# Kernel optimization log

Hardware: AMD Instinct MI355X
Metric: run time of the kernel (lower is better)

## Reference

```python
import jax, jax.numpy as jnp
import numpy as np
import math

B, L, D, H = 8, 2048, 1024, 16
DK = D // H
FACTOR = 1
TOP_K = int(FACTOR * math.log(L))  # = 7


def _linear(x, W, b):
    # torch nn.Linear: y = x @ W.T + b, W shape (out, in)
    return x @ W.T + b


def setup_inputs() -> dict:
    rng = jax.random.key(0)
    ks = jax.random.split(rng, 11)
    s = 1.0 / math.sqrt(D)
    inp = {
        "query": jax.random.normal(ks[0], (B, L, D), jnp.float32),
        "key": jax.random.normal(ks[1], (B, L, D), jnp.float32),
        "value": jax.random.normal(ks[2], (B, L, D), jnp.float32),
        "Wq": jax.random.normal(ks[3], (D, D), jnp.float32) * s,
        "bq": jnp.zeros((D,), jnp.float32),
        "Wk": jax.random.normal(ks[4], (D, D), jnp.float32) * s,
        "bk": jnp.zeros((D,), jnp.float32),
        "Wv": jax.random.normal(ks[5], (D, D), jnp.float32) * s,
        "bv": jnp.zeros((D,), jnp.float32),
        "Wo": jax.random.normal(ks[6], (D, D), jnp.float32) * s,
        "bo": jnp.zeros((D,), jnp.float32),
    }
    return inp


def _autocorrelation(q, k, v):
    # q,k,v: (B, H, DK, L)
    q_fft = jnp.fft.rfft(q, axis=-1)
    k_fft = jnp.fft.rfft(k, axis=-1)
    corr = jnp.fft.irfft(q_fft * jnp.conj(k_fft), n=L, axis=-1)  # (B,H,DK,L)

    mean_value = jnp.mean(corr, axis=2)                 # (B,H,L)
    weights, index = jax.lax.top_k(mean_value, TOP_K)   # (B,H,TOP_K)
    tmp_corr = jax.nn.softmax(weights, axis=-1)         # (B,H,TOP_K)

    t = jnp.arange(L)[None, None, :]                    # (1,1,L)
    delays_agg = jnp.zeros_like(v)
    for i in range(TOP_K):  # TOP_K=7, static small loop
        # torch.roll(v, -delay, -1)[..., t] == v[..., (t+delay) % L]
        idx = (t + index[:, :, i:i + 1]) % L            # (B,H,L)
        idx = jnp.broadcast_to(idx[:, :, None, :], v.shape)
        pattern = jnp.take_along_axis(v, idx, axis=-1)  # (B,H,DK,L)
        delays_agg = delays_agg + pattern * tmp_corr[:, :, i][:, :, None, None]
    return delays_agg, tmp_corr


def reference(query, key, value, Wq, bq, Wk, bk, Wv, bv, Wo, bo):
    residual = query
    # project and split heads -> (B, H, DK, L)
    q = _linear(query, Wq, bq).reshape(B, L, H, DK).transpose(0, 2, 3, 1)
    k = _linear(key, Wk, bk).reshape(B, L, H, DK).transpose(0, 2, 3, 1)
    v = _linear(value, Wv, bv).reshape(B, L, H, DK).transpose(0, 2, 3, 1)

    agg, corr_weights = _autocorrelation(q, k, v)       # (B,H,DK,L)
    corr_value = agg.transpose(0, 3, 1, 2).reshape(B, L, D)
    corr_value = _linear(corr_value, Wo, bo)
    # dropout in eval mode = identity
    return corr_value + residual, corr_weights
```

## Files before the change

kernel.cpp:

```cpp
#include <hip/hip_runtime.h>
#include <hip/hip_bf16.h>
#include <math.h>

#define BB   8
#define LL   2048
#define DD   1024
#define HH   16
#define DKK  64
#define TOPK 7

typedef unsigned short u16;
typedef short short8 __attribute__((ext_vector_type(8)));
typedef short s4v    __attribute__((ext_vector_type(4)));
typedef float f32x4  __attribute__((ext_vector_type(4)));
typedef int   int4v  __attribute__((ext_vector_type(4)));

#define QXH_B   0ull
#define QXL_B   16777216ull
#define KXH_B   33554432ull
#define KXL_B   50331648ull
#define VXH_B   67108864ull
#define QWH_B   100663296ull
#define QWL_B   101711872ull
#define KWH_B   102760448ull
#define KWL_B   103809024ull
#define VWH_B   104857600ull
#define OWH_B   106954752ull
#define QTB_B   109051904ull
#define KTB_B   142606336ull
#define VBF_B   176160768ull
#define PART_B  0ull
#define PART_STRIDE 2064
#define TOPW_B  16777216ull
#define TOPI_B  16780800ull

#define SX_INV  5461.3333f
#define SW_INV  174762.67f
#define CS1     6.8664551e-5f
#define CS2     2.6822090e-7f

__device__ __forceinline__ int2 xcd_swizzle_8x128() {
    const int lin = blockIdx.y * gridDim.x + blockIdx.x;
    const int swz = (lin & 7) * 128 + (lin >> 3);
    return make_int2(swz & 7, swz >> 3);
}

__device__ __forceinline__ u16 f2bf(float f) {
    unsigned u = __float_as_uint(f);
    unsigned r = u + 0x7FFFu + ((u >> 16) & 1u);
    return (u16)(r >> 16);
}
__device__ __forceinline__ float bf2f(u16 h) {
    return __uint_as_float((unsigned)h << 16);
}

__device__ __forceinline__ void split4_i8(const float* __restrict__ x,
                                          char* __restrict__ hi,
                                          char* __restrict__ lo,
                                          float inv_s, size_t i) {
    float4 t = ((const float4*)x)[i];
    float f[4] = {t.x, t.y, t.z, t.w};
    unsigned hp = 0, lp = 0;
    #pragma unroll
    for (int j = 0; j < 4; ++j) {
        int q = __float2int_rn(f[j] * inv_s);
        q = min(max(q, -32639), 32639);
        int xl = ((q + 128) & 255) - 128;
        int xh = (q - xl) >> 8;
        hp |= ((unsigned)(xh & 255)) << (8 * j);
        lp |= ((unsigned)(xl & 255)) << (8 * j);
    }
    ((unsigned*)hi)[i] = hp;
    ((unsigned*)lo)[i] = lp;
}

__device__ __forceinline__ void cvt4_bf(const float* __restrict__ x,
                                        u16* __restrict__ o, size_t i) {
    float4 t = ((const float4*)x)[i];
    s4v h;
    h[0] = (short)f2bf(t.x); h[1] = (short)f2bf(t.y);
    h[2] = (short)f2bf(t.z); h[3] = (short)f2bf(t.w);
    *(s4v*)(o + i * 4) = h;
}

__global__ __launch_bounds__(256) void k_conv_all(
    const float* __restrict__ q, const float* __restrict__ k,
    const float* __restrict__ v,
    const float* __restrict__ Wq, const float* __restrict__ Wk,
    const float* __restrict__ Wv, const float* __restrict__ Wo,
    char* __restrict__ qh, char* __restrict__ ql,
    char* __restrict__ kh, char* __restrict__ kl, u16* __restrict__ vx,
    char* __restrict__ qwh, char* __restrict__ qwl,
    char* __restrict__ kwh, char* __restrict__ kwl,
    u16* __restrict__ vwh, u16* __restrict__ owh)
{
    const int b = blockIdx.x;
    const int t = threadIdx.x;
    if (b < 16384) {
        split4_i8(q, qh, ql, SX_INV, (size_t)b * 256 + t);
    } else if (b < 32768) {
        split4_i8(k, kh, kl, SX_INV, (size_t)(b - 16384) * 256 + t);
    } else if (b < 49152) {
        cvt4_bf(v, vx, (size_t)(b - 32768) * 256 + t);
    } else if (b < 50176) {
        split4_i8(Wq, qwh, qwl, SW_INV, (size_t)(b - 49152) * 256 + t);
    } else if (b < 51200) {
        split4_i8(Wk, kwh, kwl, SW_INV, (size_t)(b - 50176) * 256 + t);
    } else if (b < 52224) {
        cvt4_bf(Wv, vwh, (size_t)(b - 51200) * 256 + t);
    } else {
        cvt4_bf(Wo, owh, (size_t)(b - 52224) * 256 + t);
    }
}

__device__ __forceinline__ void async16(u16* l, const u16* g) {
    __builtin_amdgcn_global_load_lds(
        (const __attribute__((address_space(1))) void*)g,
        (__attribute__((address_space(3))) void*)l, 16, 0, 0);
}
__device__ __forceinline__ void async16b(char* l, const char* g) {
    __builtin_amdgcn_global_load_lds(
        (const __attribute__((address_space(1))) void*)g,
        (__attribute__((address_space(3))) void*)l, 16, 0, 0);
}

__global__ __launch_bounds__(256, 2) void gemm_i8split(
    const char* __restrict__ Ah, const char* __restrict__ Al,
    const char* __restrict__ Bh, const char* __restrict__ Bl,
    const float* __restrict__ bias, u16* __restrict__ outb)
{
    __shared__ __align__(16) char lds[2][4][8192];
    const int t = threadIdx.x;
    const int w = t >> 6, lane = t & 63;
    const int2 tb = xcd_swizzle_8x128();
    const int m0 = tb.y * 128, n0 = tb.x * 128;
    const int srow = lane >> 2, sslot = lane & 3;
    const int r15 = lane & 15, kg = lane >> 4;
    const int wr = w >> 1, wc = w & 1;
    const int r4 = (lane >> 4) * 4;
    const int swzb = (kg ^ (r15 & 3)) << 4;
    const int a_off = (wr * 64 + r15) * 64 + swzb;
    const int b_off = (wc * 64 + r15) * 64 + swzb;

    int4v acc1[4][4], acc2[4][4];
    #pragma unroll
    for (int i = 0; i < 4; ++i)
        #pragma unroll
        for (int j = 0; j < 4; ++j) {
            acc1[i][j] = (int4v){0,0,0,0};
            acc2[i][j] = (int4v){0,0,0,0};
        }

    #define STAGE8(buf, kt)                                                       \
    {                                                                             \
        const int gc0 = (kt) * 64;                                                \
        _Pragma("unroll")                                                         \
        for (int i = 0; i < 2; ++i) {                                             \
            const int row  = w * 32 + i * 16 + srow;                              \
            const int kch  = (sslot ^ (row & 3)) << 4;                            \
            const int loff = w * 2048 + i * 1024;                                 \
            async16b(&lds[buf][0][loff], Ah + (size_t)(m0 + row) * 1024 + gc0 + kch); \
            async16b(&lds[buf][1][loff], Bh + (size_t)(n0 + row) * 1024 + gc0 + kch); \
            async16b(&lds[buf][2][loff], Al + (size_t)(m0 + row) * 1024 + gc0 + kch); \
            async16b(&lds[buf][3][loff], Bl + (size_t)(n0 + row) * 1024 + gc0 + kch); \
        }                                                                         \
    }

    #define COMP8(buf)                                                            \
    {                                                                             \
        const char* cb = &lds[buf][0][0];                                         \
        int4v ah[4], bh4[4], al[4], bl[4];                                        \
        _Pragma("unroll")                                                         \
        for (int mi = 0; mi < 4; ++mi) ah[mi] = *(const int4v*)(cb + a_off + mi * 1024); \
        _Pragma("unroll")                                                         \
        for (int nj = 0; nj < 4; ++nj) bh4[nj] = *(const int4v*)(cb + 8192 + b_off + nj * 1024); \
        _Pragma("unroll")                                                         \
        for (int mi = 0; mi < 4; ++mi)                                            \
            _Pragma("unroll")                                                     \
            for (int nj = 0; nj < 4; ++nj)                                        \
                acc1[mi][nj] = __builtin_amdgcn_mfma_i32_16x16x64_i8(ah[mi], bh4[nj], acc1[mi][nj], 0, 0, 0); \
        _Pragma("unroll")                                                         \
        for (int nj = 0; nj < 4; ++nj) bl[nj] = *(const int4v*)(cb + 24576 + b_off + nj * 1024); \
        _Pragma("unroll")                                                         \
        for (int mi = 0; mi < 4; ++mi)                                            \
            _Pragma("unroll")                                                     \
            for (int nj = 0; nj < 4; ++nj)                                        \
                acc2[mi][nj] = __builtin_amdgcn_mfma_i32_16x16x64_i8(ah[mi], bl[nj], acc2[mi][nj], 0, 0, 0); \
        _Pragma("unroll")                                                         \
        for (int mi = 0; mi < 4; ++mi) al[mi] = *(const int4v*)(cb + 16384 + a_off + mi * 1024); \
        _Pragma("unroll")                                                         \
        for (int mi = 0; mi < 4; ++mi)                                            \
            _Pragma("unroll")                                                     \
            for (int nj = 0; nj < 4; ++nj)                                        \
                acc2[mi][nj] = __builtin_amdgcn_mfma_i32_16x16x64_i8(al[mi], bh4[nj], acc2[mi][nj], 0, 0, 0); \
    }

    STAGE8(0, 0);
    __syncthreads();
    int cur = 0;
    for (int kt = 0; kt < 15; ++kt) {
        STAGE8(cur ^ 1, kt + 1);
        COMP8(cur);
        __syncthreads();
        cur ^= 1;
    }
    COMP8(cur);

    #pragma unroll
    for (int nj = 0; nj < 4; ++nj) {
        const int n = n0 + wc * 64 + nj * 16 + r15;
        const float bs = bias[n];
        #pragma unroll
        for (int mi = 0; mi < 4; ++mi) {
            const int m = m0 + wr * 64 + mi * 16 + r4;
            const int b = m >> 11;
            const int l = m & 2047;
            s4v v;
            #pragma unroll
            for (int r = 0; r < 4; ++r)
                v[r] = (short)f2bf(fmaf(CS1, (float)acc1[mi][nj][r],
                                   fmaf(CS2, (float)acc2[mi][nj][r], bs)));
            *(s4v*)(outb + (((size_t)((b << 10) + n)) << 11) + l) = v;
        }
    }
    #undef STAGE8
    #undef COMP8
}

template<int EPI>
__global__ __launch_bounds__(512, 2) void gemm_bf16_256(
    const u16* __restrict__ A, const u16* __restrict__ B,
    const float* __restrict__ bias, const float* __restrict__ resid,
    float* __restrict__ outp)
{
    extern __shared__ u16 ldsx[];
    u16* lsA = ldsx;
    u16* lsB = ldsx + 32768;
    const int t = threadIdx.x;
    const int wid = t >> 6, lane = t & 63;
    const int wr = wid >> 2, wc = wid & 3;
    const int r15 = lane & 15, kg = lane >> 4, r4 = kg * 4;
    const int lin = blockIdx.y * gridDim.x + blockIdx.x;
    const int swz = (lin & 7) * 32 + (lin >> 3);
    const int n0 = (swz & 3) * 256, m0 = (swz >> 2) * 256;
    const int sb = wid * 2;
    const int sr = lane >> 3;
    const int ss = lane & 7;

    #define STG(bufb, ls, rb, src, base0, kt)                                   \
    {                                                                           \
        _Pragma("unroll")                                                       \
        for (int j = 0; j < 2; ++j) {                                           \
            const int r = (rb) + (sb + j) * 8 + sr;                             \
            async16(ls + (size_t)(bufb) * 16384 + (size_t)(rb) * 64 + (size_t)(sb + j) * 512, \
                    src + (size_t)((base0) + r) * 1024 + (kt) * 64 + ((ss ^ (r & 7)) << 3)); \
        }                                                                       \
    }

    f32x4 acc[8][4];
    #pragma unroll
    for (int i = 0; i < 8; ++i)
        #pragma unroll
        for (int j = 0; j < 4; ++j)
            acc[i][j] = (f32x4){0.f, 0.f, 0.f, 0.f};

    STG(0, lsB, 0,   B, n0, 0);
    STG(0, lsB, 128, B, n0, 0);
    STG(0, lsA, 0,   A, m0, 0);
    STG(0, lsA, 128, A, m0, 0);

    for (int kt = 0; kt < 16; ++kt) {
        const int bf = kt & 1, nb = bf ^ 1;
        asm volatile("s_waitcnt vmcnt(0)" ::: "memory");
        asm volatile("s_barrier" ::: "memory");
        short8 bfr[4][2];
        #pragma unroll
        for (int nj = 0; nj < 4; ++nj)
            #pragma unroll
            for (int ks = 0; ks < 2; ++ks) {
                const int row = wc * 64 + nj * 16 + r15;
                bfr[nj][ks] = *(const short8*)(lsB + (size_t)bf * 16384 +
                    (size_t)row * 64 + ((((ks << 2) + kg) ^ (row & 7)) << 3));
            }
        #pragma unroll
        for (int p = 0; p < 4; ++p) {
            short8 afr[2][2];
            #pragma unroll
            for (int mh = 0; mh < 2; ++mh)
                #pragma unroll
                for (int ks = 0; ks < 2; ++ks) {
                    const int row = wr * 128 + (p * 2 + mh) * 16 + r15;
                    afr[mh][ks] = *(const short8*)(lsA + (size_t)bf * 16384 +
                        (size_t)row * 64 + ((((ks << 2) + kg) ^ (row & 7)) << 3));
                }
            if (kt < 15) {
                if (p == 0)      { STG(nb, lsB, 0,   B, n0, kt + 1); }
                else if (p == 1) { STG(nb, lsB, 128, B, n0, kt + 1); }
                else if (p == 2) { STG(nb, lsA, 0,   A, m0, kt + 1); }
                else             { STG(nb, lsA, 128, A, m0, kt + 1); }
            }
            asm volatile("s_barrier" ::: "memory");
            __builtin_amdgcn_s_setprio(1);
            #pragma unroll
            for (int mh = 0; mh < 2; ++mh)
                #pragma unroll
                for (int nj = 0; nj < 4; ++nj)
                    #pragma unroll
                    for (int ks = 0; ks < 2; ++ks)
                        acc[p * 2 + mh][nj] = __builtin_amdgcn_mfma_f32_16x16x32_bf16(
                            afr[mh][ks], bfr[nj][ks], acc[p * 2 + mh][nj], 0, 0, 0);
            __builtin_amdgcn_s_setprio(0);
            asm volatile("s_barrier" ::: "memory");
        }
    }

    if (EPI == 2) {
        u16* outb = (u16*)outp;
        #pragma unroll
        for (int nj = 0; nj < 4; ++nj) {
            const int n = n0 + wc * 64 + nj * 16 + r15;
            const float bs = bias[n];
            #pragma unroll
            for (int mi = 0; mi < 8; ++mi) {
                const int m = m0 + wr * 128 + mi * 16 + r4;
                const int b = m >> 11;
                const int l = m & 2047;
                s4v v;
                #pragma unroll
                for (int r = 0; r < 4; ++r) v[r] = (short)f2bf(acc[mi][nj][r] + bs);
                *(s4v*)(outb + (((size_t)((b << 10) + n)) << 11) + l) = v;
            }
        }
    } else {
        #pragma unroll
        for (int mi = 0; mi < 8; ++mi) {
            #pragma unroll
            for (int r = 0; r < 4; ++r) {
                const int m = m0 + wr * 128 + mi * 16 + r4 + r;
                const float* rrow = resid + ((size_t)m << 10);
                float* orow = outp + ((size_t)m << 10);
                #pragma unroll
                for (int nj = 0; nj < 4; ++nj) {
                    const int n = n0 + wc * 64 + nj * 16 + r15;
                    orow[n] = acc[mi][nj][r] + bias[n] + rrow[n];
                }
            }
        }
    }
    #undef STG
}

#define IDX(i) ((i) + ((i) >> 3))
#define FFT_BUF 2304

__device__ __forceinline__ float2 c_add(float2 a, float2 b){ return make_float2(a.x+b.x, a.y+b.y); }
__device__ __forceinline__ float2 c_sub(float2 a, float2 b){ return make_float2(a.x-b.x, a.y-b.y); }
__device__ __forceinline__ float2 cmul(float2 a, float2 b){
    return make_float2(fmaf(a.x, b.x, -a.y*b.y), fmaf(a.x, b.y, a.y*b.x));
}
template<bool INV>
__device__ __forceinline__ float2 rot90(float2 z) {
    return INV ? make_float2(-z.y, z.x) : make_float2(z.y, -z.x);
}

template<bool INV>
__device__ __forceinline__ void dft8(const float2* a, float2* y) {
    const float r = 0.70710678118654752f;
    float2 e0 = c_add(a[0], a[4]), e1 = c_sub(a[0], a[4]);
    float2 e2 = c_add(a[2], a[6]), e3 = rot90<INV>(c_sub(a[2], a[6]));
    float2 E0 = c_add(e0, e2), E2 = c_sub(e0, e2);
    float2 E1 = c_add(e1, e3), E3 = c_sub(e1, e3);
    float2 o0 = c_add(a[1], a[5]), o1 = c_sub(a[1], a[5]);
    float2 o2 = c_add(a[3], a[7]), o3 = rot90<INV>(c_sub(a[3], a[7]));
    float2 O0 = c_add(o0, o2), O2 = c_sub(o0, o2);
    float2 O1 = c_add(o1, o3), O3 = c_sub(o1, o3);
    float2 T1 = INV ? make_float2(r*(O1.x - O1.y), r*(O1.x + O1.y))
                    : make_float2(r*(O1.x + O1.y), r*(O1.y - O1.x));
    float2 T2 = rot90<INV>(O2);
    float2 T3 = INV ? make_float2(-r*(O3.x + O3.y), r*(O3.x - O3.y))
                    : make_float2(r*(O3.y - O3.x), -r*(O3.x + O3.y));
    y[0] = c_add(E0, O0); y[4] = c_sub(E0, O0);
    y[1] = c_add(E1, T1); y[5] = c_sub(E1, T1);
    y[2] = c_add(E2, T2); y[6] = c_sub(E2, T2);
    y[3] = c_add(E3, T3); y[7] = c_sub(E3, T3);
}

template<bool INV>
__device__ float2* fft2048_r8(float2* bufA, float2* bufB, const float2* twd, int tid)
{
    float2* src = bufA;
    float2* dst = bufB;
    #pragma unroll
    for (int st = 0; st < 3; ++st) {
        const int s = 1 << (3 * st);
        const int u = tid;
        const int sp = u & ~(s - 1);
        float2 a[8], y[8];
        #pragma unroll
        for (int t = 0; t < 8; ++t) a[t] = src[IDX(u + (t << 8))];
        dft8<INV>(a, y);
        float2 w1 = twd[sp];
        if (INV) w1.y = -w1.y;
        const int ob = u + 7 * sp;
        dst[IDX(ob)]     = y[0];
        dst[IDX(ob + s)] = cmul(y[1], w1);
        float2 w = w1;
        #pragma unroll
        for (int t = 2; t < 8; ++t) {
            w = cmul(w, w1);
            dst[IDX(ob + t * s)] = cmul(y[t], w);
        }
        __syncthreads();
        float2* tmp = src; src = dst; dst = tmp;
    }
    #pragma unroll
    for (int h = 0; h < 2; ++h) {
        const int u = tid + (h << 8);
        float2 a0 = src[IDX(u)],        a1 = src[IDX(u + 512)];
        float2 a2 = src[IDX(u + 1024)], a3 = src[IDX(u + 1536)];
        float2 b0 = c_add(a0, a2), b1 = c_sub(a0, a2);
        float2 b2 = c_add(a1, a3), b3 = rot90<INV>(c_sub(a1, a3));
        dst[IDX(u)]        = c_add(b0, b2);
        dst[IDX(u + 512)]  = c_add(b1, b3);
        dst[IDX(u + 1024)] = c_sub(b0, b2);
        dst[IDX(u + 1536)] = c_sub(b1, b3);
    }
    __syncthreads();
    return dst;
}

__global__ __launch_bounds__(256) void fft_corr_partial(
    const u16* __restrict__ qT, const u16* __restrict__ kT,
    float* __restrict__ part)
{
    __shared__ float2 bufA[FFT_BUF];
    __shared__ float2 bufB[FFT_BUF];
    __shared__ float2 twd[256];
    const int tid = threadIdx.x;
    const int blk = blockIdx.x;
    const int bh  = blk >> 3, g = blk & 7;
    {
        float s, c;
        sincosf((float)tid * 3.0679615757712823e-3f, &s, &c);
        twd[tid] = make_float2(c, -s);
    }
    float2 racc[4];
    #pragma unroll
    for (int ii = 0; ii < 4; ++ii) racc[ii] = make_float2(0.f, 0.f);
    float2 racc4 = make_float2(0.f, 0.f);

    const u16* qbase = qT + ((size_t)bh * DKK + g * 8) * LL;
    const u16* kbase = kT + ((size_t)bh * DKK + g * 8) * LL;
    for (int dd = 0; dd < 8; ++dd) {
        __syncthreads();
        const u16* qr = qbase + (size_t)dd * LL;
        const u16* kr = kbase + (size_t)dd * LL;
        short8 q8 = *(const short8*)(qr + tid * 8);
        short8 k8 = *(const short8*)(kr + tid * 8);
        #pragma unroll
        for (int j = 0; j < 8; ++j)
            bufA[IDX(tid * 8 + j)] = make_float2(bf2f((u16)q8[j]), bf2f((u16)k8[j]));
        __syncthreads();
        float2* res = fft2048_r8<false>(bufA, bufB, twd, tid);
        #pragma unroll
        for (int ii = 0; ii < 4; ++ii) {
            const int f = tid + (ii << 8);
            float2 zf = res[IDX(f)];
            float2 zc = res[IDX((2048 - f) & 2047)];
            float2 Q = make_float2(0.5f*(zf.x + zc.x), 0.5f*(zf.y - zc.y));
            float2 K = make_float2(0.5f*(zf.y + zc.y), -0.5f*(zf.x - zc.x));
            racc[ii].x += Q.x*K.x + Q.y*K.y;
            racc[ii].y += Q.y*K.x - Q.x*K.y;
        }
        if (tid == 0) {
            float2 zf = res[IDX(1024)];
            racc4.x += zf.x * zf.y;
        }
    }
    float* po = part + (size_t)blk * PART_STRIDE;
    #pragma unroll
    for (int ii = 0; ii < 4; ++ii) {
        const int f = tid + (ii << 8);
        po[2*f]     = racc[ii].x;
        po[2*f + 1] = racc[ii].y;
    }
    if (tid == 0) { po[2048] = racc4.x; po[2049] = racc4.y; }
}

__global__ __launch_bounds__(256) void fft_inv_topk(
    const float* __restrict__ part, float* __restrict__ out1,
    float* __restrict__ topw, int* __restrict__ topi)
{
    __shared__ float2 bufA[FFT_BUF];
    __shared__ float2 bufB[FFT_BUF];
    __shared__ float2 twd[256];
    __shared__ float  mv[2048];
    __shared__ float  rv[256];
    __shared__ int    ri[256];
    __shared__ float  selv[TOPK];
    __shared__ int    seli[TOPK];
    const int tid = threadIdx.x;
    const int bh  = blockIdx.x;
    {
        float s, c;
        sincosf((float)tid * 3.0679615757712823e-3f, &s, &c);
        twd[tid] = make_float2(c, -s);
    }
    for (int f = tid; f < 1025; f += 256) {
        float sx = 0.f, sy = 0.f;
        for (int g2 = 0; g2 < 8; ++g2) {
            const float* po = part + (size_t)(bh * 8 + g2) * PART_STRIDE + 2*f;
            sx += po[0]; sy += po[1];
        }
        bufA[IDX(f)] = make_float2(sx, sy);
        if (f > 0 && f < 1024) bufA[IDX(2048 - f)] = make_float2(sx, -sy);
    }
    __syncthreads();
    float2* res = fft2048_r8<true>(bufA, bufB, twd, tid);
    const float scale = 1.0f / (2048.0f * 64.0f);
    #pragma unroll
    for (int j = 0; j < 8; ++j) {
        const int l = tid + (j << 8);
        mv[l] = res[IDX(l)].x * scale;
    }
    __syncthreads();
    for (int it = 0; it < TOPK; ++it) {
        float bvv = -3.0e38f; int bii = 0;
        #pragma unroll
        for (int c = 0; c < 8; ++c) {
            const int idx = tid * 8 + c;
            const float v = mv[idx];
            if (v > bvv) { bvv = v; bii = idx; }
        }
        rv[tid] = bvv; ri[tid] = bii;
        __syncthreads();
        for (int off = 128; off > 0; off >>= 1) {
            if (tid < off) {
                const float v2 = rv[tid + off]; const int i2 = ri[tid + off];
                if (v2 > rv[tid] || (v2 == rv[tid] && i2 < ri[tid])) {
                    rv[tid] = v2; ri[tid] = i2;
                }
            }
            __syncthreads();
        }
        if (tid == 0) { selv[it] = rv[0]; seli[it] = ri[0]; mv[ri[0]] = -3.0e38f; }
        __syncthreads();
    }
    if (tid == 0) {
        const float mx = selv[0];
        float e[TOPK]; float ssum = 0.f;
        #pragma unroll
        for (int i = 0; i < TOPK; ++i) { e[i] = expf(selv[i] - mx); ssum += e[i]; }
        const float inv = 1.0f / ssum;
        #pragma unroll
        for (int i = 0; i < TOPK; ++i) {
            const float w = e[i] * inv;
            out1[bh * TOPK + i] = w;
            topw[bh * TOPK + i] = w;
            topi[bh * TOPK + i] = seli[i];
        }
    }
}

__global__ __launch_bounds__(256) void gather_tr(
    const u16* __restrict__ vbf, const float* __restrict__ topw,
    const int* __restrict__ topi, u16* __restrict__ aggrow)
{
    extern __shared__ u16 vstage[];
    __shared__ float wv[TOPK];
    __shared__ int   wi[TOPK];
    const int blk  = blockIdx.x;
    const int bh   = blk >> 1, half = blk & 1;
    const int b    = bh >> 4, h = bh & 15;
    const int tid  = threadIdx.x;
    if (tid < TOPK) {
        wv[tid] = topw[bh * TOPK + tid];
        wi[tid] = topi[bh * TOPK + tid];
    }
    const u16* vsrc = vbf + ((size_t)bh * DKK + half * 32) * LL;
    short8* vs8 = (short8*)vstage;
    #pragma unroll
    for (int k = 0; k < 32; ++k)
        vs8[tid + k * 256] = *(const short8*)(vsrc + (size_t)(tid + k * 256) * 8);
    __syncthreads();
    const int doff = h * 64 + half * 32;
    for (int c = 0; c < 8; ++c) {
        const int l = c * 256 + tid;
        u16* orow = aggrow + ((size_t)((b << 11) + l) << 10) + doff;
        short8 o[4];
        #pragma unroll
        for (int d = 0; d < 32; ++d) {
            float s = 0.f;
            #pragma unroll
            for (int i = 0; i < TOPK; ++i)
                s = fmaf(wv[i], bf2f(vstage[d * 2048 + ((l + wi[i]) & 2047)]), s);
            o[d >> 3][d & 7] = (short)f2bf(s);
        }
        #pragma unroll
        for (int q = 0; q < 4; ++q)
            *(short8*)(orow + q * 8) = o[q];
    }
}

extern "C" void kernel_launch(void* const* d_in, const int* in_sizes, int n_in,
                              void* d_out, int out_size, void* d_ws, size_t ws_size,
                              hipStream_t stream)
{
    const float* query = (const float*)d_in[0];
    const float* key   = (const float*)d_in[1];
    const float* value = (const float*)d_in[2];
    const float* Wq    = (const float*)d_in[3];
    const float* bq    = (const float*)d_in[4];
    const float* Wk    = (const float*)d_in[5];
    const float* bk    = (const float*)d_in[6];
    const float* Wv    = (const float*)d_in[7];
    const float* bv    = (const float*)d_in[8];
    const float* Wo    = (const float*)d_in[9];
    const float* bo    = (const float*)d_in[10];
    float* out = (float*)d_out;
    char*  ws  = (char*)d_ws;

    char* qxh = (char*)(ws + QXH_B);
    char* qxl = (char*)(ws + QXL_B);
    char* kxh = (char*)(ws + KXH_B);
    char* kxl = (char*)(ws + KXL_B);
    u16*  vxh = (u16*)(ws + VXH_B);
    char* qwh = (char*)(ws + QWH_B);
    char* qwl = (char*)(ws + QWL_B);
    char* kwh = (char*)(ws + KWH_B);
    char* kwl = (char*)(ws + KWL_B);
    u16*  vwh = (u16*)(ws + VWH_B);
    u16*  owh = (u16*)(ws + OWH_B);
    u16*  qTb = (u16*)(ws + QTB_B);
    u16*  kTb = (u16*)(ws + KTB_B);
    u16*  vbf = (u16*)(ws + VBF_B);
    float* part = (float*)(ws + PART_B);
    float* topw = (float*)(ws + TOPW_B);
    int*   topi = (int*)(ws + TOPI_B);
    u16*  aggrow = (u16*)(ws + QTB_B);

    dim3 gg(DD / 128, (BB * LL) / 128);
    dim3 g2(DD / 256, (BB * LL) / 256);

    k_conv_all<<<53248, 256, 0, stream>>>(query, key, value, Wq, Wk, Wv, Wo,
                                          qxh, qxl, kxh, kxl, vxh,
                                          qwh, qwl, kwh, kwl, vwh, owh);
    gemm_i8split<<<gg, 256, 0, stream>>>(qxh, qxl, qwh, qwl, bq, qTb);
    gemm_i8split<<<gg, 256, 0, stream>>>(kxh, kxl, kwh, kwl, bk, kTb);
    gemm_bf16_256<2><<<g2, 512, 131072, stream>>>(vxh, vwh, bv, nullptr, (float*)vbf);
    fft_corr_partial<<<BB * HH * 8, 256, 0, stream>>>(qTb, kTb, part);
    fft_inv_topk<<<BB * HH, 256, 0, stream>>>(part, out + 16777216, topw, topi);
    gather_tr<<<BB * HH * 2, 256, 131072, stream>>>(vbf, topw, topi, aggrow);
    gemm_bf16_256<1><<<g2, 512, 131072, stream>>>(aggrow, owh, bo, query, out);
}
```

Baseline: 363.7 us.

## Enlarge int8 split GEMM tile to 256x128 with 8 waves and interleaved staging

The Q and K projection int8-split GEMM now uses 256x128 tiles with 512 threads in place of 128x128 tiles with 256 threads, so each B tile is reused across more rows. The main loop is rewritten to split the three MFMA phases with barriers, issue the next-stage async loads between them, and raise wave priority around the MFMA blocks. This is meant to improve operand reuse and overlap of loads with compute. In exchange it needs 96KB of dynamic LDS, adds many more barriers per iteration, and launches fewer blocks.

```diff
diff --git a/kernel.cpp b/kernel.cpp
--- a/kernel.cpp
+++ b/kernel.cpp
@@ -39,12 +39,6 @@
 #define CS1     6.8664551e-5f
 #define CS2     2.6822090e-7f
 
-__device__ __forceinline__ int2 xcd_swizzle_8x128() {
-    const int lin = blockIdx.y * gridDim.x + blockIdx.x;
-    const int swz = (lin & 7) * 128 + (lin >> 3);
-    return make_int2(swz & 7, swz >> 3);
-}
-
 __device__ __forceinline__ u16 f2bf(float f) {
     unsigned u = __float_as_uint(f);
     unsigned r = u + 0x7FFFu + ((u >> 16) & 1u);
@@ -124,23 +118,30 @@
         (__attribute__((address_space(3))) void*)l, 16, 0, 0);
 }
 
-__global__ __launch_bounds__(256, 2) void gemm_i8split(
+__global__ __launch_bounds__(512, 2) void gemm_i8_256(
     const char* __restrict__ Ah, const char* __restrict__ Al,
     const char* __restrict__ Bh, const char* __restrict__ Bl,
     const float* __restrict__ bias, u16* __restrict__ outb)
 {
-    __shared__ __align__(16) char lds[2][4][8192];
+    extern __shared__ char ldsc[];
+    char* lAh = ldsc;
+    char* lAl = ldsc + 32768;
+    char* lBh = ldsc + 65536;
+    char* lBl = ldsc + 81920;
     const int t = threadIdx.x;
-    const int w = t >> 6, lane = t & 63;
-    const int2 tb = xcd_swizzle_8x128();
-    const int m0 = tb.y * 128, n0 = tb.x * 128;
-    const int srow = lane >> 2, sslot = lane & 3;
-    const int r15 = lane & 15, kg = lane >> 4;
-    const int wr = w >> 1, wc = w & 1;
-    const int r4 = (lane >> 4) * 4;
-    const int swzb = (kg ^ (r15 & 3)) << 4;
-    const int a_off = (wr * 64 + r15) * 64 + swzb;
-    const int b_off = (wc * 64 + r15) * 64 + swzb;
+    const int wid = t >> 6, lane = t & 63;
+    const int wr = wid >> 1, wc = wid & 1;
+    const int r15 = lane & 15, kg = lane >> 4, r4 = kg * 4;
+    const int lin = blockIdx.y * gridDim.x + blockIdx.x;
+    const int swz = (lin & 7) * 64 + (lin >> 3);
+    const int n0 = (swz & 7) * 128, m0 = (swz >> 3) * 256;
+
+    #define STGU(ls, bufb, bufsz, rowbase, src, base0, kt)                      \
+    {                                                                           \
+        const int r = (rowbase) + wid * 16 + (lane >> 2);                       \
+        async16b(ls + (size_t)(bufb) * (bufsz) + (size_t)(rowbase) * 64 + wid * 1024, \
+                 src + (size_t)((base0) + r) * 1024 + (kt) * 64 + (((lane & 3) ^ (r & 3)) << 4)); \
+    }
 
     int4v acc1[4][4], acc2[4][4];
     #pragma unroll
@@ -151,60 +152,87 @@
             acc2[i][j] = (int4v){0,0,0,0};
         }
 
-    #define STAGE8(buf, kt)                                                       \
-    {                                                                             \
-        const int gc0 = (kt) * 64;                                                \
-        _Pragma("unroll")                                                         \
-        for (int i = 0; i < 2; ++i) {                                             \
-            const int row  = w * 32 + i * 16 + srow;                              \
-            const int kch  = (sslot ^ (row & 3)) << 4;                            \
-            const int loff = w * 2048 + i * 1024;                                 \
-            async16b(&lds[buf][0][loff], Ah + (size_t)(m0 + row) * 1024 + gc0 + kch); \
-            async16b(&lds[buf][1][loff], Bh + (size_t)(n0 + row) * 1024 + gc0 + kch); \
-            async16b(&lds[buf][2][loff], Al + (size_t)(m0 + row) * 1024 + gc0 + kch); \
-            async16b(&lds[buf][3][loff], Bl + (size_t)(n0 + row) * 1024 + gc0 + kch); \
-        }                                                                         \
-    }
-
-    #define COMP8(buf)                                                            \
-    {                                                                             \
-        const char* cb = &lds[buf][0][0];                                         \
-        int4v ah[4], bh4[4], al[4], bl[4];                                        \
-        _Pragma("unroll")                                                         \
-        for (int mi = 0; mi < 4; ++mi) ah[mi] = *(const int4v*)(cb + a_off + mi * 1024); \
-        _Pragma("unroll")                                                         \
-        for (int nj = 0; nj < 4; ++nj) bh4[nj] = *(const int4v*)(cb + 8192 + b_off + nj * 1024); \
-        _Pragma("unroll")                                                         \
-        for (int mi = 0; mi < 4; ++mi)                                            \
-            _Pragma("unroll")                                                     \
-            for (int nj = 0; nj < 4; ++nj)                                        \
-                acc1[mi][nj] = __builtin_amdgcn_mfma_i32_16x16x64_i8(ah[mi], bh4[nj], acc1[mi][nj], 0, 0, 0); \
-        _Pragma("unroll")                                                         \
-        for (int nj = 0; nj < 4; ++nj) bl[nj] = *(const int4v*)(cb + 24576 + b_off + nj * 1024); \
-        _Pragma("unroll")                                                         \
-        for (int mi = 0; mi < 4; ++mi)                                            \
-            _Pragma("unroll")                                                     \
-            for (int nj = 0; nj < 4; ++nj)                                        \
-                acc2[mi][nj] = __builtin_amdgcn_mfma_i32_16x16x64_i8(ah[mi], bl[nj], acc2[mi][nj], 0, 0, 0); \
-        _Pragma("unroll")                                                         \
-        for (int mi = 0; mi < 4; ++mi) al[mi] = *(const int4v*)(cb + 16384 + a_off + mi * 1024); \
-        _Pragma("unroll")                                                         \
-        for (int mi = 0; mi < 4; ++mi)                                            \
-            _Pragma("unroll")                                                     \
-            for (int nj = 0; nj < 4; ++nj)                                        \
-                acc2[mi][nj] = __builtin_amdgcn_mfma_i32_16x16x64_i8(al[mi], bh4[nj], acc2[mi][nj], 0, 0, 0); \
-    }
-
-    STAGE8(0, 0);
-    __syncthreads();
-    int cur = 0;
-    for (int kt = 0; kt < 15; ++kt) {
-        STAGE8(cur ^ 1, kt + 1);
-        COMP8(cur);
-        __syncthreads();
-        cur ^= 1;
-    }
-    COMP8(cur);
+    STGU(lAh, 0, 16384, 0,   Ah, m0, 0);
+    STGU(lAh, 0, 16384, 128, Ah, m0, 0);
+    STGU(lAl, 0, 16384, 0,   Al, m0, 0);
+    STGU(lAl, 0, 16384, 128, Al, m0, 0);
+    STGU(lBh, 0, 8192,  0,   Bh, n0, 0);
+    STGU(lBl, 0, 8192,  0,   Bl, n0, 0);
+
+    for (int kt = 0; kt < 16; ++kt) {
+        const int bf = kt & 1, nb = bf ^ 1;
+        asm volatile("s_waitcnt vmcnt(0)" ::: "memory");
+        asm volatile("s_barrier" ::: "memory");
+        int4v ah[4], bh4[4];
+        #pragma unroll
+        for (int mi = 0; mi < 4; ++mi) {
+            const int row = wr * 64 + mi * 16 + r15;
+            ah[mi] = *(const int4v*)(lAh + (size_t)bf * 16384 +
+                      (size_t)row * 64 + ((kg ^ (r15 & 3)) << 4));
+        }
+        #pragma unroll
+        for (int nj = 0; nj < 4; ++nj) {
+            const int row = wc * 64 + nj * 16 + r15;
+            bh4[nj] = *(const int4v*)(lBh + (size_t)bf * 8192 +
+                       (size_t)row * 64 + ((kg ^ (r15 & 3)) << 4));
+        }
+        if (kt < 15) {
+            STGU(lAh, nb, 16384, 0,   Ah, m0, kt + 1);
+            STGU(lAh, nb, 16384, 128, Ah, m0, kt + 1);
+        }
+        asm volatile("s_barrier" ::: "memory");
+        __builtin_amdgcn_s_setprio(1);
+        #pragma unroll
+        for (int mi = 0; mi < 4; ++mi)
+            #pragma unroll
+            for (int nj = 0; nj < 4; ++nj)
+                acc1[mi][nj] = __builtin_amdgcn_mfma_i32_16x16x64_i8(
+                    ah[mi], bh4[nj], acc1[mi][nj], 0, 0, 0);
+        __builtin_amdgcn_s_setprio(0);
+        asm volatile("s_barrier" ::: "memory");
+        int4v bl4[4];
+        #pragma unroll
+        for (int nj = 0; nj < 4; ++nj) {
+            const int row = wc * 64 + nj * 16 + r15;
+            bl4[nj] = *(const int4v*)(lBl + (size_t)bf * 8192 +
+                       (size_t)row * 64 + ((kg ^ (r15 & 3)) << 4));
+        }
+        if (kt < 15) {
+            STGU(lAl, nb, 16384, 0,   Al, m0, kt + 1);
+            STGU(lAl, nb, 16384, 128, Al, m0, kt + 1);
+        }
+        asm volatile("s_barrier" ::: "memory");
+        __builtin_amdgcn_s_setprio(1);
+        #pragma unroll
+        for (int mi = 0; mi < 4; ++mi)
+            #pragma unroll
+            for (int nj = 0; nj < 4; ++nj)
+                acc2[mi][nj] = __builtin_amdgcn_mfma_i32_16x16x64_i8(
+                    ah[mi], bl4[nj], acc2[mi][nj], 0, 0, 0);
+        __builtin_amdgcn_s_setprio(0);
+        asm volatile("s_barrier" ::: "memory");
+        int4v al[4];
+        #pragma unroll
+        for (int mi = 0; mi < 4; ++mi) {
+            const int row = wr * 64 + mi * 16 + r15;
+            al[mi] = *(const int4v*)(lAl + (size_t)bf * 16384 +
+                      (size_t)row * 64 + ((kg ^ (r15 & 3)) << 4));
+        }
+        if (kt < 15) {
+            STGU(lBh, nb, 8192, 0, Bh, n0, kt + 1);
+            STGU(lBl, nb, 8192, 0, Bl, n0, kt + 1);
+        }
+        asm volatile("s_barrier" ::: "memory");
+        __builtin_amdgcn_s_setprio(1);
+        #pragma unroll
+        for (int mi = 0; mi < 4; ++mi)
+            #pragma unroll
+            for (int nj = 0; nj < 4; ++nj)
+                acc2[mi][nj] = __builtin_amdgcn_mfma_i32_16x16x64_i8(
+                    al[mi], bh4[nj], acc2[mi][nj], 0, 0, 0);
+        __builtin_amdgcn_s_setprio(0);
+        asm volatile("s_barrier" ::: "memory");
+    }
 
     #pragma unroll
     for (int nj = 0; nj < 4; ++nj) {
@@ -223,8 +251,7 @@
             *(s4v*)(outb + (((size_t)((b << 10) + n)) << 11) + l) = v;
         }
     }
-    #undef STAGE8
-    #undef COMP8
+    #undef STGU
 }
 
 template<int EPI>
@@ -639,14 +666,14 @@
     int*   topi = (int*)(ws + TOPI_B);
     u16*  aggrow = (u16*)(ws + QTB_B);
 
-    dim3 gg(DD / 128, (BB * LL) / 128);
     dim3 g2(DD / 256, (BB * LL) / 256);
+    dim3 g3(DD / 128, (BB * LL) / 256);
 
     k_conv_all<<<53248, 256, 0, stream>>>(query, key, value, Wq, Wk, Wv, Wo,
                                           qxh, qxl, kxh, kxl, vxh,
                                           qwh, qwl, kwh, kwl, vwh, owh);
-    gemm_i8split<<<gg, 256, 0, stream>>>(qxh, qxl, qwh, qwl, bq, qTb);
-    gemm_i8split<<<gg, 256, 0, stream>>>(kxh, kxl, kwh, kwl, bk, kTb);
+    gemm_i8_256<<<g3, 512, 98304, stream>>>(qxh, qxl, qwh, qwl, bq, qTb);
+    gemm_i8_256<<<g3, 512, 98304, stream>>>(kxh, kxl, kwh, kwl, bk, kTb);
     gemm_bf16_256<2><<<g2, 512, 131072, stream>>>(vxh, vwh, bv, nullptr, (float*)vbf);
     fft_corr_partial<<<BB * HH * 8, 256, 0, stream>>>(qTb, kTb, part);
     fft_inv_topk<<<BB * HH, 256, 0, stream>>>(part, out + 16777216, topw, topi);
```

After: 364.1 us. About the same (+0.1%).
